# Kernel tuning notes

Hardware: AMD Instinct MI355X
Metric: run time of the kernel (lower is better)

## Reference

```python
import jax, jax.numpy as jnp
import numpy as np

BITS = 4
MAXQ = 15            # 2**BITS - 1
PACK = 32 // BITS    # 8 int4 values per int32
GROUPSIZE = 128
M, K, N = 2048, 4096, 4096
G = K // GROUPSIZE


def setup_inputs() -> dict:
    key = jax.random.key(0)
    k1, k2, k3, k4, k5 = jax.random.split(key, 5)
    x = jax.random.normal(k1, (M, K), dtype=jnp.float32)
    qweight = jax.random.randint(k2, (K // PACK, N), 0, 2147483647, dtype=jnp.int32)
    qzeros = jax.random.randint(k3, (G, N // PACK), 0, 2147483647, dtype=jnp.int32)
    scales = jax.random.uniform(k4, (G, N), dtype=jnp.float32) * 0.01
    g_idx = (jnp.arange(K, dtype=jnp.int32) // GROUPSIZE).astype(jnp.int32)
    bias = jax.random.normal(k5, (N,), dtype=jnp.float32)
    return {"x": x, "qweight": qweight, "qzeros": qzeros,
            "scales": scales, "g_idx": g_idx, "bias": bias}


def _dequantize(qweight, qzeros, scales, g_idx):
    shifts = (jnp.arange(PACK, dtype=jnp.int32) * BITS)
    # unpack weights along K: [K//8, N] -> [K//8, 8, N] -> [K, N]
    w_int = ((qweight[:, None, :] >> shifts[None, :, None]) & MAXQ)
    w_int = w_int.reshape(K, N)
    # unpack zeros along N: [G, N//8] -> [G, N//8, 8] -> [G, N]; kernel adds 1
    z_int = ((qzeros[:, :, None] >> shifts[None, None, :]) & MAXQ) + 1
    z_int = z_int.reshape(G, N)
    # group-wise dequant: W[k, n] = (w - zeros[g_idx[k]]) * scales[g_idx[k]]
    W = (w_int - z_int[g_idx]).astype(jnp.float32) * scales[g_idx]
    return W  # [K, N]


def reference(x, qweight, qzeros, scales, g_idx, bias):
    W = _dequantize(qweight, qzeros, scales, g_idx)
    return x @ W + bias  # [M, N]
```

## Files before the change

### kernel.cpp

```cpp
#include <hip/hip_runtime.h>
#include <hip/hip_bf16.h>
#include <stdint.h>

#define M_DIM 2048
#define K_DIM 4096
#define N_DIM 4096

typedef __attribute__((ext_vector_type(8))) short short8;
typedef __attribute__((ext_vector_type(4))) float f32x4;

#define MFMA __builtin_amdgcn_mfma_f32_16x16x32_bf16

__device__ __forceinline__ uint32_t bf16pk(float a, float b) {
  uint32_t ua = __float_as_uint(a);
  ua = (ua + 0x7FFFu + ((ua >> 16) & 1u)) >> 16;
  uint32_t ub = __float_as_uint(b);
  ub = (ub + 0x7FFFu + ((ub >> 16) & 1u)) >> 16;
  return ua | (ub << 16);
}

__device__ __forceinline__ void glds16(const char* g, char* l) {
  __builtin_amdgcn_global_load_lds((__attribute__((address_space(1))) void*)g,
                                   (__attribute__((address_space(3))) void*)l, 16, 0, 0);
}


__global__ void __launch_bounds__(256) prep_kernel(const float* __restrict__ x,
                                                   const uint32_t* __restrict__ qweight,
                                                   const uint32_t* __restrict__ qzeros,
                                                   const float* __restrict__ scales,
                                                   char* __restrict__ xImg,
                                                   char* __restrict__ wImg) {
  const int tid = threadIdx.x;
  if (blockIdx.x < 1024) {
    const int bid = blockIdx.x;
    const int mt = bid >> 6, ktp = bid & 63;
    const int row = tid & 127, sh = tid >> 7;
    const int s = ktp * 2 + sh;
    const float* src = x + (size_t)(mt * 128 + row) * K_DIM + s * 32;
    char* dst = xImg + (size_t)(mt * 128 + s) * 8192 + row * 16;
#pragma unroll
    for (int slot = 0; slot < 4; ++slot) {
      float4 f0 = *(const float4*)(src + slot * 8);
      float4 f1 = *(const float4*)(src + slot * 8 + 4);
      uint4 pk;
      pk.x = bf16pk(f0.x, f0.y);
      pk.y = bf16pk(f0.z, f0.w);
      pk.z = bf16pk(f1.x, f1.y);
      pk.w = bf16pk(f1.z, f1.w);
      *(uint4*)(dst + slot * 2048) = pk;
    }
  } else {
    const int bid = blockIdx.x - 1024;
    const int nt = bid >> 6, ktp = bid & 63;
    const int n = tid & 127, sh = tid >> 7;
    const int s = ktp * 2 + sh;
    const int g = ktp >> 1;
    const int gn = nt * 128 + n;
    uint32_t zq = qzeros[g * (N_DIM / 8) + (gn >> 3)];
    const int z = (int)((zq >> ((gn & 7) * 4)) & 15u) + 1;
    const float s_ = scales[g * N_DIM + gn];
    char* dst = wImg + (size_t)(nt * 128 + s) * 8192 + n * 16;
#pragma unroll
    for (int slot = 0; slot < 4; ++slot) {
      uint32_t q = qweight[(size_t)(s * 4 + slot) * N_DIM + gn];
      float f[8];
#pragma unroll
      for (int v = 0; v < 8; ++v) {
        int w = (int)((q >> (4 * v)) & 15u);
        f[v] = (float)(w - z) * s_;
      }
      uint4 pk;
      pk.x = bf16pk(f[0], f[1]);
      pk.y = bf16pk(f[2], f[3]);
      pk.z = bf16pk(f[4], f[5]);
      pk.w = bf16pk(f[6], f[7]);
      *(uint4*)(dst + slot * 2048) = pk;
    }
  }
}

__global__ void __launch_bounds__(256, 2) gemm_kernel(const char* __restrict__ xImg,
                                                      const char* __restrict__ wImg,
                                                      const float* __restrict__ bias,
                                                      float* __restrict__ out) {
  __shared__ uint4 ldsv[4096];
  char* lds = (char*)ldsv;
  const int tid = threadIdx.x;
  const int lane = tid & 63, wid = tid >> 6;
  const int ks = wid >> 1, wc = wid & 1;
  const int lr = lane & 15, lk = lane >> 4;

  const int bid = blockIdx.x;
  const int wg = (bid & 7) * 64 + (bid >> 3);
  const int mb = wg & 15, nb = wg >> 4;

  f32x4 acc[8][4];
#pragma unroll
  for (int i = 0; i < 8; ++i)
#pragma unroll
    for (int j = 0; j < 4; ++j) acc[i][j] = f32x4{0.f, 0.f, 0.f, 0.f};

  const char* aT0 = xImg + (size_t)mb * 128 * 8192;
  const char* aT1 = aT0 + (size_t)64 * 8192;
  const char* bW = wImg + (size_t)(nb * 128 + ks * 64) * 8192 + lk * 2048 + (wc * 64 + lr) * 16;

  int aoff[8];
#pragma unroll
  for (int i = 0; i < 8; ++i) aoff[i] = ks * 8192 + lk * 2048 + (i * 16 + lr) * 16;

#define STAGE(T, SB)                                                     \
  do {                                                                   \
    char* d = lds + (SB);                                                \
    const char* sa0 = aT0 + (size_t)(T) * 8192;                          \
    const char* sa1 = aT1 + (size_t)(T) * 8192;                          \
    glds16(sa0 + tid * 16, d + tid * 16);                                \
    glds16(sa0 + 4096 + tid * 16, d + 4096 + tid * 16);                  \
    glds16(sa1 + tid * 16, d + 8192 + tid * 16);                         \
    glds16(sa1 + 4096 + tid * 16, d + 12288 + tid * 16);                 \
  } while (0)

  STAGE(0, 0);
  asm volatile("s_waitcnt vmcnt(0)" ::: "memory");
  __builtin_amdgcn_sched_barrier(0);
  __builtin_amdgcn_s_barrier();

#pragma unroll 2
  for (int t = 0; t < 64; ++t) {
    const char* buf = lds + (t & 1) * 16384;
    const char* bS = bW + (size_t)t * 8192;

    short8 b0 = *(const short8*)(bS);
    short8 b1 = *(const short8*)(bS + 256);
    short8 b2 = *(const short8*)(bS + 512);
    short8 b3 = *(const short8*)(bS + 768);
    if (t < 63) STAGE(t + 1, ((t + 1) & 1) * 16384);
    __builtin_amdgcn_sched_barrier(0);

    short8 a0 = *(const short8*)(buf + aoff[0]);
    short8 a1 = *(const short8*)(buf + aoff[1]);
    short8 a2 = *(const short8*)(buf + aoff[2]);
    short8 a3 = *(const short8*)(buf + aoff[3]);
    short8 a4 = *(const short8*)(buf + aoff[4]);
    short8 a5 = *(const short8*)(buf + aoff[5]);
    short8 a6 = *(const short8*)(buf + aoff[6]);
    short8 a7 = *(const short8*)(buf + aoff[7]);

    asm volatile("s_waitcnt lgkmcnt(4)" ::: "memory");
    __builtin_amdgcn_sched_barrier(0);
    __builtin_amdgcn_s_setprio(1);
    acc[0][0] = MFMA(a0, b0, acc[0][0], 0, 0, 0);
    acc[1][0] = MFMA(a1, b0, acc[1][0], 0, 0, 0);
    acc[2][0] = MFMA(a2, b0, acc[2][0], 0, 0, 0);
    acc[3][0] = MFMA(a3, b0, acc[3][0], 0, 0, 0);
    acc[0][1] = MFMA(a0, b1, acc[0][1], 0, 0, 0);
    acc[1][1] = MFMA(a1, b1, acc[1][1], 0, 0, 0);
    acc[2][1] = MFMA(a2, b1, acc[2][1], 0, 0, 0);
    acc[3][1] = MFMA(a3, b1, acc[3][1], 0, 0, 0);
    acc[0][2] = MFMA(a0, b2, acc[0][2], 0, 0, 0);
    acc[1][2] = MFMA(a1, b2, acc[1][2], 0, 0, 0);
    acc[2][2] = MFMA(a2, b2, acc[2][2], 0, 0, 0);
    acc[3][2] = MFMA(a3, b2, acc[3][2], 0, 0, 0);
    acc[0][3] = MFMA(a0, b3, acc[0][3], 0, 0, 0);
    acc[1][3] = MFMA(a1, b3, acc[1][3], 0, 0, 0);
    acc[2][3] = MFMA(a2, b3, acc[2][3], 0, 0, 0);
    acc[3][3] = MFMA(a3, b3, acc[3][3], 0, 0, 0);
    asm volatile("s_waitcnt lgkmcnt(0)" ::: "memory");
    __builtin_amdgcn_sched_barrier(0);
    acc[4][0] = MFMA(a4, b0, acc[4][0], 0, 0, 0);
    acc[5][0] = MFMA(a5, b0, acc[5][0], 0, 0, 0);
    acc[6][0] = MFMA(a6, b0, acc[6][0], 0, 0, 0);
    acc[7][0] = MFMA(a7, b0, acc[7][0], 0, 0, 0);
    acc[4][1] = MFMA(a4, b1, acc[4][1], 0, 0, 0);
    acc[5][1] = MFMA(a5, b1, acc[5][1], 0, 0, 0);
    acc[6][1] = MFMA(a6, b1, acc[6][1], 0, 0, 0);
    acc[7][1] = MFMA(a7, b1, acc[7][1], 0, 0, 0);
    acc[4][2] = MFMA(a4, b2, acc[4][2], 0, 0, 0);
    acc[5][2] = MFMA(a5, b2, acc[5][2], 0, 0, 0);
    acc[6][2] = MFMA(a6, b2, acc[6][2], 0, 0, 0);
    acc[7][2] = MFMA(a7, b2, acc[7][2], 0, 0, 0);
    acc[4][3] = MFMA(a4, b3, acc[4][3], 0, 0, 0);
    acc[5][3] = MFMA(a5, b3, acc[5][3], 0, 0, 0);
    acc[6][3] = MFMA(a6, b3, acc[6][3], 0, 0, 0);
    acc[7][3] = MFMA(a7, b3, acc[7][3], 0, 0, 0);
    __builtin_amdgcn_s_setprio(0);

    if (t < 63) {
      asm volatile("s_waitcnt vmcnt(0)" ::: "memory");
      __builtin_amdgcn_sched_barrier(0);
      __builtin_amdgcn_s_barrier();
    }
  }
#undef STAGE

  __syncthreads();
  if (ks == 1) {
#pragma unroll
    for (int i = 0; i < 4; ++i)
#pragma unroll
      for (int j = 0; j < 4; ++j)
        *(f32x4*)(lds + (wc * 16 + i * 4 + j) * 1024 + lane * 16) = acc[i][j];
  } else {
#pragma unroll
    for (int i = 4; i < 8; ++i)
#pragma unroll
      for (int j = 0; j < 4; ++j)
        *(f32x4*)(lds + 32768 + (wc * 16 + (i - 4) * 4 + j) * 1024 + lane * 16) = acc[i][j];
  }
  __syncthreads();

  const int colB = nb * 128 + wc * 64 + lr;
  if (ks == 0) {
#pragma unroll
    for (int j = 0; j < 4; ++j) {
      int col = colB + j * 16;
      float bj = bias[col];
#pragma unroll
      for (int i = 0; i < 4; ++i) {
        f32x4 p = *(const f32x4*)(lds + (wc * 16 + i * 4 + j) * 1024 + lane * 16);
        int row = mb * 128 + i * 16 + lk * 4;
#pragma unroll
        for (int r = 0; r < 4; ++r)
          out[(size_t)(row + r) * N_DIM + col] = acc[i][j][r] + p[r] + bj;
      }
    }
  } else {
#pragma unroll
    for (int j = 0; j < 4; ++j) {
      int col = colB + j * 16;
      float bj = bias[col];
#pragma unroll
      for (int i = 4; i < 8; ++i) {
        f32x4 p = *(const f32x4*)(lds + 32768 + (wc * 16 + (i - 4) * 4 + j) * 1024 + lane * 16);
        int row = mb * 128 + i * 16 + lk * 4;
#pragma unroll
        for (int r = 0; r < 4; ++r)
          out[(size_t)(row + r) * N_DIM + col] = acc[i][j][r] + p[r] + bj;
      }
    }
  }
}

__global__ void fallback_kernel(const float* __restrict__ x, const uint32_t* __restrict__ qweight,
                                const uint32_t* __restrict__ qzeros, const float* __restrict__ scales,
                                const float* __restrict__ bias, float* __restrict__ out) {
  __shared__ float xs[16][17];
  __shared__ float ws[16][17];
  int tx = threadIdx.x, ty = threadIdx.y;
  int col = blockIdx.x * 16 + tx;
  int row = blockIdx.y * 16 + ty;
  float acc = 0.f;
  for (int k0 = 0; k0 < K_DIM; k0 += 16) {
    xs[ty][tx] = x[(size_t)row * K_DIM + k0 + tx];
    int k = k0 + ty;
    int g = k >> 7;
    uint32_t q = qweight[(size_t)(k >> 3) * N_DIM + col];
    int w = (int)((q >> ((k & 7) * 4)) & 15u);
    uint32_t zq = qzeros[g * (N_DIM / 8) + (col >> 3)];
    int z = (int)((zq >> ((col & 7) * 4)) & 15u) + 1;
    ws[ty][tx] = (float)(w - z) * scales[g * N_DIM + col];
    __syncthreads();
#pragma unroll
    for (int kk = 0; kk < 16; ++kk) acc += xs[ty][kk] * ws[kk][tx];
    __syncthreads();
  }
  out[(size_t)row * N_DIM + col] = acc + bias[col];
}

extern "C" void kernel_launch(void* const* d_in, const int* in_sizes, int n_in,
                              void* d_out, int out_size, void* d_ws, size_t ws_size,
                              hipStream_t stream) {
  const float* x = (const float*)d_in[0];
  const uint32_t* qweight = (const uint32_t*)d_in[1];
  const uint32_t* qzeros = (const uint32_t*)d_in[2];
  const float* scales = (const float*)d_in[3];
  const float* bias = (const float*)d_in[5];
  float* out = (float*)d_out;

  const size_t X_IMG = (size_t)16 * 128 * 8192;
  const size_t W_IMG = (size_t)32 * 128 * 8192;

  if (ws_size >= X_IMG + W_IMG) {
    char* xImg = (char*)d_ws;
    char* wImg = (char*)d_ws + X_IMG;
    prep_kernel<<<3072, 256, 0, stream>>>(x, qweight, qzeros, scales, xImg, wImg);
    gemm_kernel<<<512, 256, 0, stream>>>(xImg, wImg, bias, out);
  } else {
    fallback_kernel<<<dim3(N_DIM / 16, M_DIM / 16), dim3(16, 16), 0, stream>>>(
        x, qweight, qzeros, scales, bias, out);
  }
}
```

Before: 82.44 us.

## Widen GEMM tile to 128x256 with LDS-staged B and triple buffering

Each workgroup now runs 512 threads (8 waves) over a 128x256 output tile, so it launches 256 workgroups instead of 512. The B operand is staged through LDS alongside A instead of being read directly from global memory by each wave. A three-slot LDS ring with register double-buffering lets the LDS reads for the next step overlap the current MFMAs, and the block-to-XCD mapping is changed to share tiles across an XCD. This cuts global traffic per FLOP and hides latency better, at the cost of 144 KB of LDS, one workgroup per CU, and fewer workgroups than a full wave of the machine's CUs.

New measurement: 84.62 us. 1.03x slower.

```diff
diff --git a/kernel.cpp b/kernel.cpp
--- a/kernel.cpp
+++ b/kernel.cpp
@@ -80,20 +80,21 @@
   }
 }
 
-__global__ void __launch_bounds__(256, 2) gemm_kernel(const char* __restrict__ xImg,
+__global__ void __launch_bounds__(512, 1) gemm_kernel(const char* __restrict__ xImg,
                                                       const char* __restrict__ wImg,
                                                       const float* __restrict__ bias,
                                                       float* __restrict__ out) {
-  __shared__ uint4 ldsv[4096];
+  __shared__ uint4 ldsv[9216];
   char* lds = (char*)ldsv;
   const int tid = threadIdx.x;
   const int lane = tid & 63, wid = tid >> 6;
-  const int ks = wid >> 1, wc = wid & 1;
+  const int ks = wid >> 2, wc = wid & 3;
   const int lr = lane & 15, lk = lane >> 4;
 
   const int bid = blockIdx.x;
-  const int wg = (bid & 7) * 64 + (bid >> 3);
-  const int mb = wg & 15, nb = wg >> 4;
+  const int local = bid >> 3, xcd = bid & 7;
+  const int nb = xcd * 2 + (local & 1);
+  const int mb = local >> 1;
 
   f32x4 acc[8][4];
 #pragma unroll
@@ -101,88 +102,69 @@
 #pragma unroll
     for (int j = 0; j < 4; ++j) acc[i][j] = f32x4{0.f, 0.f, 0.f, 0.f};
 
-  const char* aT0 = xImg + (size_t)mb * 128 * 8192;
-  const char* aT1 = aT0 + (size_t)64 * 8192;
-  const char* bW = wImg + (size_t)(nb * 128 + ks * 64) * 8192 + lk * 2048 + (wc * 64 + lr) * 16;
-
-  int aoff[8];
+  const char* aT = xImg + (size_t)mb * 128 * 8192;
+  const char* bT0 = wImg + (size_t)(2 * nb) * 128 * 8192;
+  const char* bT1 = wImg + (size_t)(2 * nb + 1) * 128 * 8192;
+
+  int aoff[8], boff[4];
 #pragma unroll
   for (int i = 0; i < 8; ++i) aoff[i] = ks * 8192 + lk * 2048 + (i * 16 + lr) * 16;
-
-#define STAGE(T, SB)                                                     \
-  do {                                                                   \
-    char* d = lds + (SB);                                                \
-    const char* sa0 = aT0 + (size_t)(T) * 8192;                          \
-    const char* sa1 = aT1 + (size_t)(T) * 8192;                          \
-    glds16(sa0 + tid * 16, d + tid * 16);                                \
-    glds16(sa0 + 4096 + tid * 16, d + 4096 + tid * 16);                  \
-    glds16(sa1 + tid * 16, d + 8192 + tid * 16);                         \
-    glds16(sa1 + 4096 + tid * 16, d + 12288 + tid * 16);                 \
+#pragma unroll
+  for (int j = 0; j < 4; ++j)
+    boff[j] = 16384 + ks * 16384 + (wc >> 1) * 8192 + lk * 2048 +
+              ((wc & 1) * 64 + j * 16 + lr) * 16;
+
+#define STAGE(T, SLOT)                                                     \
+  do {                                                                     \
+    char* d = lds + (SLOT) * 49152;                                        \
+    glds16(aT + (size_t)(T) * 8192 + tid * 16, d + tid * 16);              \
+    glds16(aT + (size_t)(64 + (T)) * 8192 + tid * 16, d + 8192 + tid * 16);\
+    glds16(bT0 + (size_t)(T) * 8192 + tid * 16, d + 16384 + tid * 16);     \
+    glds16(bT1 + (size_t)(T) * 8192 + tid * 16, d + 24576 + tid * 16);     \
+    glds16(bT0 + (size_t)(64 + (T)) * 8192 + tid * 16, d + 32768 + tid * 16);\
+    glds16(bT1 + (size_t)(64 + (T)) * 8192 + tid * 16, d + 40960 + tid * 16);\
   } while (0)
+
+  short8 vA[2][8], vB[2][4];
 
   STAGE(0, 0);
   asm volatile("s_waitcnt vmcnt(0)" ::: "memory");
   __builtin_amdgcn_sched_barrier(0);
   __builtin_amdgcn_s_barrier();
+#pragma unroll
+  for (int i = 0; i < 8; ++i) vA[0][i] = *(const short8*)(lds + aoff[i]);
+#pragma unroll
+  for (int j = 0; j < 4; ++j) vB[0][j] = *(const short8*)(lds + boff[j]);
+  STAGE(1, 1);
+  asm volatile("s_waitcnt vmcnt(0)" ::: "memory");
+  __builtin_amdgcn_sched_barrier(0);
+  __builtin_amdgcn_s_barrier();
 
 #pragma unroll 2
   for (int t = 0; t < 64; ++t) {
-    const char* buf = lds + (t & 1) * 16384;
-    const char* bS = bW + (size_t)t * 8192;
-
-    short8 b0 = *(const short8*)(bS);
-    short8 b1 = *(const short8*)(bS + 256);
-    short8 b2 = *(const short8*)(bS + 512);
-    short8 b3 = *(const short8*)(bS + 768);
-    if (t < 63) STAGE(t + 1, ((t + 1) & 1) * 16384);
+    const int cs = t & 1, ns = cs ^ 1;
+
+    if (t < 63) {
+      const char* rbuf = lds + ((t + 1) % 3) * 49152;
+#pragma unroll
+      for (int i = 0; i < 8; ++i) vA[ns][i] = *(const short8*)(rbuf + aoff[i]);
+#pragma unroll
+      for (int j = 0; j < 4; ++j) vB[ns][j] = *(const short8*)(rbuf + boff[j]);
+    }
+    if (t < 62) STAGE(t + 2, (t + 2) % 3);
     __builtin_amdgcn_sched_barrier(0);
 
-    short8 a0 = *(const short8*)(buf + aoff[0]);
-    short8 a1 = *(const short8*)(buf + aoff[1]);
-    short8 a2 = *(const short8*)(buf + aoff[2]);
-    short8 a3 = *(const short8*)(buf + aoff[3]);
-    short8 a4 = *(const short8*)(buf + aoff[4]);
-    short8 a5 = *(const short8*)(buf + aoff[5]);
-    short8 a6 = *(const short8*)(buf + aoff[6]);
-    short8 a7 = *(const short8*)(buf + aoff[7]);
-
-    asm volatile("s_waitcnt lgkmcnt(4)" ::: "memory");
+    if (t < 63) asm volatile("s_waitcnt lgkmcnt(12)" ::: "memory");
+    else        asm volatile("s_waitcnt lgkmcnt(0)" ::: "memory");
     __builtin_amdgcn_sched_barrier(0);
+
     __builtin_amdgcn_s_setprio(1);
-    acc[0][0] = MFMA(a0, b0, acc[0][0], 0, 0, 0);
-    acc[1][0] = MFMA(a1, b0, acc[1][0], 0, 0, 0);
-    acc[2][0] = MFMA(a2, b0, acc[2][0], 0, 0, 0);
-    acc[3][0] = MFMA(a3, b0, acc[3][0], 0, 0, 0);
-    acc[0][1] = MFMA(a0, b1, acc[0][1], 0, 0, 0);
-    acc[1][1] = MFMA(a1, b1, acc[1][1], 0, 0, 0);
-    acc[2][1] = MFMA(a2, b1, acc[2][1], 0, 0, 0);
-    acc[3][1] = MFMA(a3, b1, acc[3][1], 0, 0, 0);
-    acc[0][2] = MFMA(a0, b2, acc[0][2], 0, 0, 0);
-    acc[1][2] = MFMA(a1, b2, acc[1][2], 0, 0, 0);
-    acc[2][2] = MFMA(a2, b2, acc[2][2], 0, 0, 0);
-    acc[3][2] = MFMA(a3, b2, acc[3][2], 0, 0, 0);
-    acc[0][3] = MFMA(a0, b3, acc[0][3], 0, 0, 0);
-    acc[1][3] = MFMA(a1, b3, acc[1][3], 0, 0, 0);
-    acc[2][3] = MFMA(a2, b3, acc[2][3], 0, 0, 0);
-    acc[3][3] = MFMA(a3, b3, acc[3][3], 0, 0, 0);
-    asm volatile("s_waitcnt lgkmcnt(0)" ::: "memory");
-    __builtin_amdgcn_sched_barrier(0);
-    acc[4][0] = MFMA(a4, b0, acc[4][0], 0, 0, 0);
-    acc[5][0] = MFMA(a5, b0, acc[5][0], 0, 0, 0);
-    acc[6][0] = MFMA(a6, b0, acc[6][0], 0, 0, 0);
-    acc[7][0] = MFMA(a7, b0, acc[7][0], 0, 0, 0);
-    acc[4][1] = MFMA(a4, b1, acc[4][1], 0, 0, 0);
-    acc[5][1] = MFMA(a5, b1, acc[5][1], 0, 0, 0);
-    acc[6][1] = MFMA(a6, b1, acc[6][1], 0, 0, 0);
-    acc[7][1] = MFMA(a7, b1, acc[7][1], 0, 0, 0);
-    acc[4][2] = MFMA(a4, b2, acc[4][2], 0, 0, 0);
-    acc[5][2] = MFMA(a5, b2, acc[5][2], 0, 0, 0);
-    acc[6][2] = MFMA(a6, b2, acc[6][2], 0, 0, 0);
-    acc[7][2] = MFMA(a7, b2, acc[7][2], 0, 0, 0);
-    acc[4][3] = MFMA(a4, b3, acc[4][3], 0, 0, 0);
-    acc[5][3] = MFMA(a5, b3, acc[5][3], 0, 0, 0);
-    acc[6][3] = MFMA(a6, b3, acc[6][3], 0, 0, 0);
-    acc[7][3] = MFMA(a7, b3, acc[7][3], 0, 0, 0);
+#pragma unroll
+    for (int j = 0; j < 4; ++j) {
+#pragma unroll
+      for (int i = 0; i < 8; ++i)
+        acc[i][j] = MFMA(vA[cs][i], vB[cs][j], acc[i][j], 0, 0, 0);
+    }
     __builtin_amdgcn_s_setprio(0);
 
     if (t < 63) {
@@ -205,11 +187,11 @@
     for (int i = 4; i < 8; ++i)
 #pragma unroll
       for (int j = 0; j < 4; ++j)
-        *(f32x4*)(lds + 32768 + (wc * 16 + (i - 4) * 4 + j) * 1024 + lane * 16) = acc[i][j];
+        *(f32x4*)(lds + 65536 + (wc * 16 + (i - 4) * 4 + j) * 1024 + lane * 16) = acc[i][j];
   }
   __syncthreads();
 
-  const int colB = nb * 128 + wc * 64 + lr;
+  const int colB = nb * 256 + wc * 64 + lr;
   if (ks == 0) {
 #pragma unroll
     for (int j = 0; j < 4; ++j) {
@@ -231,7 +213,7 @@
       float bj = bias[col];
 #pragma unroll
       for (int i = 4; i < 8; ++i) {
-        f32x4 p = *(const f32x4*)(lds + 32768 + (wc * 16 + (i - 4) * 4 + j) * 1024 + lane * 16);
+        f32x4 p = *(const f32x4*)(lds + 65536 + (wc * 16 + (i - 4) * 4 + j) * 1024 + lane * 16);
         int row = mb * 128 + i * 16 + lk * 4;
 #pragma unroll
         for (int r = 0; r < 4; ++r)
@@ -284,7 +266,7 @@
     char* xImg = (char*)d_ws;
     char* wImg = (char*)d_ws + X_IMG;
     prep_kernel<<<3072, 256, 0, stream>>>(x, qweight, qzeros, scales, xImg, wImg);
-    gemm_kernel<<<512, 256, 0, stream>>>(xImg, wImg, bias, out);
+    gemm_kernel<<<256, 512, 0, stream>>>(xImg, wImg, bias, out);
   } else {
     fallback_kernel<<<dim3(N_DIM / 16, M_DIM / 16), dim3(16, 16), 0, stream>>>(
         x, qweight, qzeros, scales, bias, out);
```
